# Kernel optimization log

Measured on AMD Instinct MI355X. Metric: run time of the kernel, lower is better.

Reference implementation:

```python
import jax, jax.numpy as jnp
import numpy as np

NEG = 10000.0

def setup_inputs() -> dict:
    key = jax.random.key(0)
    ks = jax.random.split(key, 5)
    B, S, D = 2, 2048, 1024
    std = 1.0 / np.sqrt(D)
    return {
        "x": jax.random.normal(ks[0], (B, S, D), dtype=jnp.float32),
        "Wq": jax.random.normal(ks[1], (D, D), dtype=jnp.float32) * std,
        "bq": jnp.zeros((D,), jnp.float32),
        "Wk": jax.random.normal(ks[2], (D, D), dtype=jnp.float32) * std,
        "bk": jnp.zeros((D,), jnp.float32),
        "Wv": jax.random.normal(ks[3], (D, D), dtype=jnp.float32) * std,
        "bv": jnp.zeros((D,), jnp.float32),
        "Wo": jax.random.normal(ks[4], (D, D), dtype=jnp.float32) * std,
        "bo": jnp.zeros((D,), jnp.float32),
    }

def reference(x, Wq, bq, Wk, bk, Wv, bv, Wo, bo):
    # Linear projections + relu activation (as in the keras layer; note: no head split
    # is performed in this implementation, head_num is only a divisibility check).
    q = jax.nn.relu(x @ Wq + bq)  # [B,S,D]
    k = jax.nn.relu(x @ Wk + bk)
    v = jax.nn.relu(x @ Wv + bv)
    D = q.shape[-1]
    e = jnp.einsum('bqd,bkd->bqk', q, k) / jnp.sqrt(jnp.float32(D))  # [B,S,S]
    # history_only causal mask: penalize key positions j > query position i
    S = e.shape[-1]
    causal = (jnp.arange(S)[None, :] > jnp.arange(S)[:, None]).astype(e.dtype)
    e = e - NEG * causal[None, :, :]
    # stable softmax exactly as in the source (max-subtract, exp, normalize)
    e = jnp.exp(e - jnp.max(e, axis=-1, keepdims=True))
    attn = e / jnp.sum(e, axis=-1, keepdims=True)
    y = jnp.einsum('bqk,bkd->bqd', attn, v)
    return jax.nn.relu(y @ Wo + bo)
```

## Files before the change

kernel.cpp:

```cpp
#include <hip/hip_runtime.h>
#include <math.h>


typedef _Float16 f16x8 __attribute__((ext_vector_type(8)));
typedef float f32x4 __attribute__((ext_vector_type(4)));

#define BK 32

__device__ __forceinline__ void gload_lds16(const void* g, void* l) {
  __builtin_amdgcn_global_load_lds(
      (const __attribute__((address_space(1))) void*)g,
      (__attribute__((address_space(3))) void*)l, 16, 0, 0);
}

template<int TMp, int TNp>
__device__ __forceinline__ void gemm_acc(
    const _Float16* __restrict__ A, const _Float16* __restrict__ BT,
    _Float16* Ah, _Float16* Bh, int sAr, int sBr, int kend, int m0, int n0,
    f32x4 (&acc)[TMp / 32][TNp / 32])
{
  const int tid  = threadIdx.x;
  const int lane = tid & 63;
  const int wid  = tid >> 6;
  const int wm   = (wid >> 1) * (TMp / 2);
  const int wn   = (wid & 1) * (TNp / 2);
  const int l15  = lane & 15;
  const int quad = lane >> 4;
  constexpr int MT = TMp / 32;
  constexpr int NT = TNp / 32;
  constexpr int AI = TMp / 64;
  constexpr int BI = TNp / 64;
  const int r16 = lane >> 2;
  const int swc = ((lane & 3) ^ ((lane >> 3) & 3)) * 8;
  const int arow = wid * (TMp / 4);
  const int brow = wid * (TNp / 4);

  for (int k0 = 0; k0 < kend; k0 += BK) {
    #pragma unroll
    for (int t = 0; t < AI; ++t)
      gload_lds16(A + (long long)(m0 + arow + t * 16 + r16) * sAr + k0 + swc,
                  Ah + (arow + t * 16) * BK);
    #pragma unroll
    for (int t = 0; t < BI; ++t)
      gload_lds16(BT + (long long)(n0 + brow + t * 16 + r16) * sBr + k0 + swc,
                  Bh + (brow + t * 16) * BK);
    __syncthreads();

    const int ch = (quad ^ ((l15 >> 1) & 3)) * 8;
    const _Float16* ab = Ah + (wm + l15) * BK + ch;
    const _Float16* bb = Bh + (wn + l15) * BK + ch;
    f16x8 af[MT], bf[NT];
    #pragma unroll
    for (int t = 0; t < MT; ++t) af[t] = *(const f16x8*)(ab + t * 16 * BK);
    #pragma unroll
    for (int t = 0; t < NT; ++t) bf[t] = *(const f16x8*)(bb + t * 16 * BK);
    #pragma unroll
    for (int mt = 0; mt < MT; ++mt)
      #pragma unroll
      for (int nt = 0; nt < NT; ++nt)
        acc[mt][nt] = __builtin_amdgcn_mfma_f32_16x16x32_f16(
            af[mt], bf[nt], acc[mt][nt], 0, 0, 0);
    __syncthreads();
  }
}

template<int TMp, int TNp, bool RELU, bool HAS_BIAS, typename OT>
__device__ __forceinline__ void gemm_store(
    f32x4 (&acc)[TMp / 32][TNp / 32], const float* __restrict__ bias,
    OT* __restrict__ C, int Nout, float scale, int m0, int n0)
{
  const int tid  = threadIdx.x;
  const int lane = tid & 63;
  const int wid  = tid >> 6;
  const int wm   = (wid >> 1) * (TMp / 2);
  const int wn   = (wid & 1) * (TNp / 2);
  const int l15  = lane & 15;
  const int quad = lane >> 4;
  constexpr int MT = TMp / 32;
  constexpr int NT = TNp / 32;

  float bvals[NT];
  if (HAS_BIAS) {
    #pragma unroll
    for (int nt = 0; nt < NT; ++nt)
      bvals[nt] = bias[n0 + wn + nt * 16 + l15];
  }
  #pragma unroll
  for (int mt = 0; mt < MT; ++mt) {
    #pragma unroll
    for (int nt = 0; nt < NT; ++nt) {
      const int col = n0 + wn + nt * 16 + l15;
      #pragma unroll
      for (int r = 0; r < 4; ++r) {
        const int row = m0 + wm + mt * 16 + quad * 4 + r;
        float v = acc[mt][nt][r] * scale;
        if (HAS_BIAS) v += bvals[nt];
        if (RELU) v = fmaxf(v, 0.f);
        C[(long long)row * Nout + col] = (OT)v;
      }
    }
  }
}

__global__ __launch_bounds__(256) void qkv_kernel(
    const _Float16* __restrict__ xh, const _Float16* __restrict__ Wcat,
    const float* __restrict__ bq, const float* __restrict__ bk,
    const float* __restrict__ bv,
    _Float16* __restrict__ Qh, _Float16* __restrict__ Kh,
    _Float16* __restrict__ Vh, int D)
{
  __shared__ _Float16 Ah[128 * BK];
  __shared__ _Float16 Bh[128 * BK];
  const int m0  = blockIdx.y * 128;
  const int n0g = blockIdx.x * 128;
  f32x4 acc[4][4];
  #pragma unroll
  for (int i = 0; i < 4; ++i)
    #pragma unroll
    for (int j = 0; j < 4; ++j) acc[i][j] = (f32x4){0.f, 0.f, 0.f, 0.f};

  gemm_acc<128, 128>(xh, Wcat, Ah, Bh, D, D, D, m0, n0g, acc);

  const int mat = n0g >> 10;
  const int c0  = n0g & 1023;
  _Float16* C = (mat == 0) ? Qh : (mat == 1) ? Kh : Vh;
  const float* bias = (mat == 0) ? bq : (mat == 1) ? bk : bv;
  gemm_store<128, 128, true, true, _Float16>(acc, bias, C, D, 1.0f, m0, c0);
}

__global__ __launch_bounds__(256) void mid_kernel(
    const _Float16* __restrict__ Qh, const _Float16* __restrict__ Kh,
    _Float16* __restrict__ E, const _Float16* __restrict__ WoT,
    const _Float16* __restrict__ Vh, _Float16* __restrict__ VWT,
    int S, int D)
{
  __shared__ _Float16 Ah[128 * BK];
  __shared__ _Float16 Bh[128 * BK];
  const _Float16 *A, *BT;
  _Float16* C;
  int m0, n0;
  float scale;
  const int id = blockIdx.x;
  if (id < 272) {
    const int z = (id >= 136);
    const int t = id - z * 136;
    int i = (int)((sqrtf(8.f * t + 1.f) - 1.f) * 0.5f);
    while ((i + 1) * (i + 2) / 2 <= t) ++i;
    while (i * (i + 1) / 2 > t) --i;
    const int j = t - i * (i + 1) / 2;
    m0 = i * 128;
    n0 = j * 128;
    A  = Qh + (long long)z * S * D;
    BT = Kh + (long long)z * S * D;
    C  = E + (long long)z * S * S;
    scale = 0.03125f;
  } else {
    const int t = id - 272;
    const int z = t >> 7;
    const int u = t & 127;
    m0 = (u >> 4) * 128;
    n0 = (u & 15) * 128;
    A  = WoT;
    BT = Vh + (long long)z * S * D;
    C  = VWT + (long long)z * D * S;
    scale = 1.0f;
  }
  f32x4 acc[4][4];
  #pragma unroll
  for (int i = 0; i < 4; ++i)
    #pragma unroll
    for (int j = 0; j < 4; ++j) acc[i][j] = (f32x4){0.f, 0.f, 0.f, 0.f};

  gemm_acc<128, 128>(A, BT, Ah, Bh, D, D, D, m0, n0, acc);
  gemm_store<128, 128, false, false, _Float16>(acc, nullptr, C, S, scale, m0, n0);
}

__global__ __launch_bounds__(256) void pv_kernel(
    const _Float16* __restrict__ E, const _Float16* __restrict__ VWT,
    const float* __restrict__ bo, float* __restrict__ out, int S, int D)
{
  __shared__ _Float16 Ah[64 * BK];
  __shared__ _Float16 Bh[128 * BK];
  const int z  = blockIdx.z;
  const int m0 = ((int)gridDim.y - 1 - (int)blockIdx.y) * 64;
  const int n0 = blockIdx.x * 128;
  const _Float16* A  = E + (long long)z * S * S;
  const _Float16* BT = VWT + (long long)z * D * S;
  float* C = out + (long long)z * S * D;
  const int kend = m0 + 64;

  f32x4 acc[2][4];
  #pragma unroll
  for (int i = 0; i < 2; ++i)
    #pragma unroll
    for (int j = 0; j < 4; ++j) acc[i][j] = (f32x4){0.f, 0.f, 0.f, 0.f};

  gemm_acc<64, 128>(A, BT, Ah, Bh, S, S, kend, m0, n0, acc);
  gemm_store<64, 128, true, true, float>(acc, bo, C, D, 1.0f, m0, n0);
}

__global__ __launch_bounds__(256) void prep_kernel(
    const float* __restrict__ x, _Float16* __restrict__ xh,
    const float* __restrict__ W0, const float* __restrict__ W1,
    const float* __restrict__ W2, const float* __restrict__ W3,
    _Float16* __restrict__ Wcat, int D)
{
  const int id = blockIdx.x;
  const int tid = threadIdx.x;
  if (id < 2048) {
    const long long i = ((long long)id * 256 + tid) * 8;
    float4 a = *(const float4*)(x + i);
    float4 b = *(const float4*)(x + i + 4);
    f16x8 o = {(_Float16)a.x, (_Float16)a.y, (_Float16)a.z, (_Float16)a.w,
               (_Float16)b.x, (_Float16)b.y, (_Float16)b.z, (_Float16)b.w};
    *(f16x8*)(xh + i) = o;
    return;
  }
  __shared__ _Float16 t[64][72];
  const int u = id - 2048;
  const int z = u >> 8;
  const int v = u & 255;
  const float* W = (z == 0) ? W0 : (z == 1) ? W1 : (z == 2) ? W2 : W3;
  _Float16* dst = Wcat + (long long)z * D * D;
  const int k0 = (v >> 4) * 64, n0 = (v & 15) * 64;
  #pragma unroll
  for (int it = 0; it < 4; ++it) {
    int idx = tid + it * 256;
    int r = idx >> 4, c4 = (idx & 15) << 2;
    float4 w = *(const float4*)(W + (long long)(k0 + r) * D + n0 + c4);
    t[r][c4 + 0] = (_Float16)w.x; t[r][c4 + 1] = (_Float16)w.y;
    t[r][c4 + 2] = (_Float16)w.z; t[r][c4 + 3] = (_Float16)w.w;
  }
  __syncthreads();
  #pragma unroll
  for (int it = 0; it < 2; ++it) {
    int idx = tid + it * 256;
    int r = idx >> 3, c8 = (idx & 7) << 3;
    f16x8 o;
    #pragma unroll
    for (int j = 0; j < 8; ++j) o[j] = t[c8 + j][r];
    *(f16x8*)(dst + (long long)(n0 + r) * D + k0 + c8) = o;
  }
}

__global__ __launch_bounds__(256) void softmax_causal_h(
    _Float16* __restrict__ E, int S)
{
  const int i = blockIdx.x;
  _Float16* row = E + ((long long)blockIdx.y * S + i) * S;
  const int tid = threadIdx.x;
  const int n = i + 1;
  const int j0 = tid * 8;

  f16x8 hv = *(const f16x8*)(row + j0);
  float vals[8];
  float m = -3.0e38f;
  #pragma unroll
  for (int t = 0; t < 8; ++t) {
    float v = (j0 + t < n) ? (float)hv[t] : -3.0e38f;
    vals[t] = v;
    m = fmaxf(m, v);
  }
  #pragma unroll
  for (int o = 32; o > 0; o >>= 1) m = fmaxf(m, __shfl_down(m, o, 64));

  __shared__ float rmax[4];
  __shared__ float rsum[4];
  const int wave = tid >> 6;
  if ((tid & 63) == 0) rmax[wave] = m;
  __syncthreads();
  m = fmaxf(fmaxf(rmax[0], rmax[1]), fmaxf(rmax[2], rmax[3]));

  float s = 0.f;
  #pragma unroll
  for (int t = 0; t < 8; ++t) {
    float e = (j0 + t < n) ? expf(vals[t] - m) : 0.f;
    vals[t] = e;
    s += e;
  }
  #pragma unroll
  for (int o = 32; o > 0; o >>= 1) s += __shfl_down(s, o, 64);
  if ((tid & 63) == 0) rsum[wave] = s;
  __syncthreads();
  s = rsum[0] + rsum[1] + rsum[2] + rsum[3];

  const float inv = 1.0f / s;
  f16x8 ov;
  #pragma unroll
  for (int t = 0; t < 8; ++t) ov[t] = (_Float16)(vals[t] * inv);
  *(f16x8*)(row + j0) = ov;
}

extern "C" void kernel_launch(void* const* d_in, const int* in_sizes, int n_in,
                              void* d_out, int out_size, void* d_ws, size_t ws_size,
                              hipStream_t stream) {
  const float* x  = (const float*)d_in[0];
  const float* Wq = (const float*)d_in[1];
  const float* bq = (const float*)d_in[2];
  const float* Wk = (const float*)d_in[3];
  const float* bk = (const float*)d_in[4];
  const float* Wv = (const float*)d_in[5];
  const float* bv = (const float*)d_in[6];
  const float* Wo = (const float*)d_in[7];
  const float* bo = (const float*)d_in[8];
  float* out = (float*)d_out;

  const int Bn = 2, S = 2048, D = 1024;
  const int M = Bn * S;
  const size_t MD = (size_t)M * D;
  const size_t DD = (size_t)D * D;
  const size_t SS = (size_t)Bn * S * S;

  _Float16* ws   = (_Float16*)d_ws;
  _Float16* xh   = ws;
  _Float16* Wcat = xh + MD;
  _Float16* Qh   = Wcat + 4 * DD;
  _Float16* Kh   = Qh + MD;
  _Float16* Vh   = Kh + MD;
  _Float16* VWT  = Vh + MD;
  _Float16* E    = VWT + MD;

  dim3 blk(256);

  prep_kernel<<<dim3(3072), blk, 0, stream>>>(x, xh, Wq, Wk, Wv, Wo, Wcat, D);

  qkv_kernel<<<dim3(3 * D / 128, M / 128), blk, 0, stream>>>(
      xh, Wcat, bq, bk, bv, Qh, Kh, Vh, D);

  mid_kernel<<<dim3(528), blk, 0, stream>>>(
      Qh, Kh, E, Wcat + 3 * DD, Vh, VWT, S, D);

  softmax_causal_h<<<dim3(S, Bn), blk, 0, stream>>>(E, S);

  pv_kernel<<<dim3(D / 128, S / 64, Bn), blk, 0, stream>>>(
      E, VWT, bo, out, S, D);
}
```

Baseline: 207.4 us.

## Double GEMM K-tile to 64 with new LDS swizzle; grid-stride mid kernel

Raises the K step of the shared GEMM loop from 32 to 64, which halves the barrier count and issues two MFMA k-slices per staged tile. The global-to-LDS load mapping and XOR swizzle are redone for the wider 128-byte rows. The mid kernel now launches 512 blocks and loops over 528 tiles with a grid stride, so 16 blocks run a second tile instead of a tail wave. The cost is double the LDS per block, which may lower occupancy, plus some load imbalance from the blocks that run two tiles.

```diff
diff --git a/kernel.cpp b/kernel.cpp
--- a/kernel.cpp
+++ b/kernel.cpp
@@ -5,7 +5,7 @@
 typedef _Float16 f16x8 __attribute__((ext_vector_type(8)));
 typedef float f32x4 __attribute__((ext_vector_type(4)));
 
-#define BK 32
+#define BK 64
 
 __device__ __forceinline__ void gload_lds16(const void* g, void* l) {
   __builtin_amdgcn_global_load_lds(
@@ -28,38 +28,46 @@
   const int quad = lane >> 4;
   constexpr int MT = TMp / 32;
   constexpr int NT = TNp / 32;
-  constexpr int AI = TMp / 64;
-  constexpr int BI = TNp / 64;
-  const int r16 = lane >> 2;
-  const int swc = ((lane & 3) ^ ((lane >> 3) & 3)) * 8;
+  constexpr int AI = TMp / 32;
+  constexpr int BI = TNp / 32;
+  const int r8  = lane >> 3;
+  const int swc = ((lane & 7) ^ r8) * 8;
   const int arow = wid * (TMp / 4);
   const int brow = wid * (TNp / 4);
 
   for (int k0 = 0; k0 < kend; k0 += BK) {
     #pragma unroll
     for (int t = 0; t < AI; ++t)
-      gload_lds16(A + (long long)(m0 + arow + t * 16 + r16) * sAr + k0 + swc,
-                  Ah + (arow + t * 16) * BK);
+      gload_lds16(A + (long long)(m0 + arow + t * 8 + r8) * sAr + k0 + swc,
+                  Ah + (arow + t * 8) * BK);
     #pragma unroll
     for (int t = 0; t < BI; ++t)
-      gload_lds16(BT + (long long)(n0 + brow + t * 16 + r16) * sBr + k0 + swc,
-                  Bh + (brow + t * 16) * BK);
+      gload_lds16(BT + (long long)(n0 + brow + t * 8 + r8) * sBr + k0 + swc,
+                  Bh + (brow + t * 8) * BK);
     __syncthreads();
 
-    const int ch = (quad ^ ((l15 >> 1) & 3)) * 8;
-    const _Float16* ab = Ah + (wm + l15) * BK + ch;
-    const _Float16* bb = Bh + (wn + l15) * BK + ch;
-    f16x8 af[MT], bf[NT];
-    #pragma unroll
-    for (int t = 0; t < MT; ++t) af[t] = *(const f16x8*)(ab + t * 16 * BK);
-    #pragma unroll
-    for (int t = 0; t < NT; ++t) bf[t] = *(const f16x8*)(bb + t * 16 * BK);
-    #pragma unroll
-    for (int mt = 0; mt < MT; ++mt)
+    const int c0 = (quad ^ (l15 & 7)) * 8;
+    const _Float16* ar = Ah + (wm + l15) * BK;
+    const _Float16* br = Bh + (wn + l15) * BK;
+    f16x8 af[MT][2], bf[NT][2];
+    #pragma unroll
+    for (int t = 0; t < MT; ++t) {
+      af[t][0] = *(const f16x8*)(ar + t * 16 * BK + c0);
+      af[t][1] = *(const f16x8*)(ar + t * 16 * BK + (c0 ^ 32));
+    }
+    #pragma unroll
+    for (int t = 0; t < NT; ++t) {
+      bf[t][0] = *(const f16x8*)(br + t * 16 * BK + c0);
+      bf[t][1] = *(const f16x8*)(br + t * 16 * BK + (c0 ^ 32));
+    }
+    #pragma unroll
+    for (int ks = 0; ks < 2; ++ks)
       #pragma unroll
-      for (int nt = 0; nt < NT; ++nt)
-        acc[mt][nt] = __builtin_amdgcn_mfma_f32_16x16x32_f16(
-            af[mt], bf[nt], acc[mt][nt], 0, 0, 0);
+      for (int mt = 0; mt < MT; ++mt)
+        #pragma unroll
+        for (int nt = 0; nt < NT; ++nt)
+          acc[mt][nt] = __builtin_amdgcn_mfma_f32_16x16x32_f16(
+              af[mt][ks], bf[nt][ks], acc[mt][nt], 0, 0, 0);
     __syncthreads();
   }
 }
@@ -136,43 +144,45 @@
 {
   __shared__ _Float16 Ah[128 * BK];
   __shared__ _Float16 Bh[128 * BK];
-  const _Float16 *A, *BT;
-  _Float16* C;
-  int m0, n0;
-  float scale;
-  const int id = blockIdx.x;
-  if (id < 272) {
-    const int z = (id >= 136);
-    const int t = id - z * 136;
-    int i = (int)((sqrtf(8.f * t + 1.f) - 1.f) * 0.5f);
-    while ((i + 1) * (i + 2) / 2 <= t) ++i;
-    while (i * (i + 1) / 2 > t) --i;
-    const int j = t - i * (i + 1) / 2;
-    m0 = i * 128;
-    n0 = j * 128;
-    A  = Qh + (long long)z * S * D;
-    BT = Kh + (long long)z * S * D;
-    C  = E + (long long)z * S * S;
-    scale = 0.03125f;
-  } else {
-    const int t = id - 272;
-    const int z = t >> 7;
-    const int u = t & 127;
-    m0 = (u >> 4) * 128;
-    n0 = (u & 15) * 128;
-    A  = WoT;
-    BT = Vh + (long long)z * S * D;
-    C  = VWT + (long long)z * D * S;
-    scale = 1.0f;
-  }
-  f32x4 acc[4][4];
-  #pragma unroll
-  for (int i = 0; i < 4; ++i)
-    #pragma unroll
-    for (int j = 0; j < 4; ++j) acc[i][j] = (f32x4){0.f, 0.f, 0.f, 0.f};
-
-  gemm_acc<128, 128>(A, BT, Ah, Bh, D, D, D, m0, n0, acc);
-  gemm_store<128, 128, false, false, _Float16>(acc, nullptr, C, S, scale, m0, n0);
+  for (int id = blockIdx.x; id < 528; id += 512) {
+    const _Float16 *A, *BT;
+    _Float16* C;
+    int m0, n0;
+    float scale;
+    if (id < 272) {
+      const int z = (id >= 136);
+      const int t = id - z * 136;
+      int i = (int)((sqrtf(8.f * t + 1.f) - 1.f) * 0.5f);
+      while ((i + 1) * (i + 2) / 2 <= t) ++i;
+      while (i * (i + 1) / 2 > t) --i;
+      const int j = t - i * (i + 1) / 2;
+      m0 = i * 128;
+      n0 = j * 128;
+      A  = Qh + (long long)z * S * D;
+      BT = Kh + (long long)z * S * D;
+      C  = E + (long long)z * S * S;
+      scale = 0.03125f;
+    } else {
+      const int t = id - 272;
+      const int z = t >> 7;
+      const int u = t & 127;
+      m0 = (u >> 4) * 128;
+      n0 = (u & 15) * 128;
+      A  = WoT;
+      BT = Vh + (long long)z * S * D;
+      C  = VWT + (long long)z * D * S;
+      scale = 1.0f;
+    }
+    f32x4 acc[4][4];
+    #pragma unroll
+    for (int i = 0; i < 4; ++i)
+      #pragma unroll
+      for (int j = 0; j < 4; ++j) acc[i][j] = (f32x4){0.f, 0.f, 0.f, 0.f};
+
+    gemm_acc<128, 128>(A, BT, Ah, Bh, D, D, D, m0, n0, acc);
+    gemm_store<128, 128, false, false, _Float16>(acc, nullptr, C, S, scale,
+                                                 m0, n0);
+  }
 }
 
 __global__ __launch_bounds__(256) void pv_kernel(
@@ -327,7 +337,7 @@
   qkv_kernel<<<dim3(3 * D / 128, M / 128), blk, 0, stream>>>(
       xh, Wcat, bq, bk, bv, Qh, Kh, Vh, D);
 
-  mid_kernel<<<dim3(528), blk, 0, stream>>>(
+  mid_kernel<<<dim3(512), blk, 0, stream>>>(
       Qh, Kh, E, Wcat + 3 * DD, Vh, VWT, S, D);
 
   softmax_causal_h<<<dim3(S, Bn), blk, 0, stream>>>(E, S);
```

Result: no change. 203.6 us (-1.8%).

## Double-buffer LDS tiles to overlap global loads with MFMA compute

Applied to the files above, without the earlier changes.

Splits the shared-memory A/B tiles into two buffers in every GEMM kernel. The next K-slice is issued with global_load_lds while MFMAs consume the current buffer, leaving one barrier per iteration instead of two. This aims to hide global-memory latency behind compute, at the cost of twice the LDS per block, which can lower occupancy.

```diff
diff --git a/kernel.cpp b/kernel.cpp
--- a/kernel.cpp
+++ b/kernel.cpp
@@ -35,20 +35,28 @@
   const int arow = wid * (TMp / 4);
   const int brow = wid * (TNp / 4);
 
-  for (int k0 = 0; k0 < kend; k0 += BK) {
+  auto stage = [&](int k0, int buf) {
+    _Float16* Ad = Ah + buf * (TMp * BK);
+    _Float16* Bd = Bh + buf * (TNp * BK);
     #pragma unroll
     for (int t = 0; t < AI; ++t)
       gload_lds16(A + (long long)(m0 + arow + t * 16 + r16) * sAr + k0 + swc,
-                  Ah + (arow + t * 16) * BK);
+                  Ad + (arow + t * 16) * BK);
     #pragma unroll
     for (int t = 0; t < BI; ++t)
       gload_lds16(BT + (long long)(n0 + brow + t * 16 + r16) * sBr + k0 + swc,
-                  Bh + (brow + t * 16) * BK);
-    __syncthreads();
+                  Bd + (brow + t * 16) * BK);
+  };
+
+  stage(0, 0);
+  __syncthreads();
+  int cur = 0;
+  for (int k0 = 0; k0 < kend; k0 += BK) {
+    if (k0 + BK < kend) stage(k0 + BK, cur ^ 1);
 
     const int ch = (quad ^ ((l15 >> 1) & 3)) * 8;
-    const _Float16* ab = Ah + (wm + l15) * BK + ch;
-    const _Float16* bb = Bh + (wn + l15) * BK + ch;
+    const _Float16* ab = Ah + cur * (TMp * BK) + (wm + l15) * BK + ch;
+    const _Float16* bb = Bh + cur * (TNp * BK) + (wn + l15) * BK + ch;
     f16x8 af[MT], bf[NT];
     #pragma unroll
     for (int t = 0; t < MT; ++t) af[t] = *(const f16x8*)(ab + t * 16 * BK);
@@ -60,7 +68,9 @@
       for (int nt = 0; nt < NT; ++nt)
         acc[mt][nt] = __builtin_amdgcn_mfma_f32_16x16x32_f16(
             af[mt], bf[nt], acc[mt][nt], 0, 0, 0);
+
     __syncthreads();
+    cur ^= 1;
   }
 }
 
@@ -109,8 +119,8 @@
     _Float16* __restrict__ Qh, _Float16* __restrict__ Kh,
     _Float16* __restrict__ Vh, int D)
 {
-  __shared__ _Float16 Ah[128 * BK];
-  __shared__ _Float16 Bh[128 * BK];
+  __shared__ _Float16 Ah[2 * 128 * BK];
+  __shared__ _Float16 Bh[2 * 128 * BK];
   const int m0  = blockIdx.y * 128;
   const int n0g = blockIdx.x * 128;
   f32x4 acc[4][4];
@@ -134,8 +144,8 @@
     const _Float16* __restrict__ Vh, _Float16* __restrict__ VWT,
     int S, int D)
 {
-  __shared__ _Float16 Ah[128 * BK];
-  __shared__ _Float16 Bh[128 * BK];
+  __shared__ _Float16 Ah[2 * 128 * BK];
+  __shared__ _Float16 Bh[2 * 128 * BK];
   const _Float16 *A, *BT;
   _Float16* C;
   int m0, n0;
@@ -172,15 +182,16 @@
     for (int j = 0; j < 4; ++j) acc[i][j] = (f32x4){0.f, 0.f, 0.f, 0.f};
 
   gemm_acc<128, 128>(A, BT, Ah, Bh, D, D, D, m0, n0, acc);
-  gemm_store<128, 128, false, false, _Float16>(acc, nullptr, C, S, scale, m0, n0);
+  gemm_store<128, 128, false, false, _Float16>(acc, nullptr, C, S, scale,
+                                               m0, n0);
 }
 
 __global__ __launch_bounds__(256) void pv_kernel(
     const _Float16* __restrict__ E, const _Float16* __restrict__ VWT,
     const float* __restrict__ bo, float* __restrict__ out, int S, int D)
 {
-  __shared__ _Float16 Ah[64 * BK];
-  __shared__ _Float16 Bh[128 * BK];
+  __shared__ _Float16 Ah[2 * 64 * BK];
+  __shared__ _Float16 Bh[2 * 128 * BK];
   const int z  = blockIdx.z;
   const int m0 = ((int)gridDim.y - 1 - (int)blockIdx.y) * 64;
   const int n0 = blockIdx.x * 128;
```

Measured after the change: 199.8 us. 1.04x faster.
